# Kernel tuning notes

Measured on AMD Instinct MI355X. Metric: run time of the kernel, lower is better.

Reference implementation:

```python
import jax, jax.numpy as jnp
import numpy as np
import math

B, TQ, TK, C, H, DFF = 4, 1024, 1024, 1024, 16, 4096
DK = C // H
EPS = 1e-12


def _mha(x_q, x_kv, wq, bq, wk, bk, wv, bv, wo, bo, mask):
    Bq, Tq, Cq = x_q.shape
    Tk = x_kv.shape[1]
    q = (x_q @ wq + bq).reshape(Bq, Tq, H, DK).transpose(0, 2, 1, 3)  # [B,H,Tq,dk]
    k = (x_kv @ wk + bk).reshape(Bq, Tk, H, DK).transpose(0, 2, 1, 3)
    v = (x_kv @ wv + bv).reshape(Bq, Tk, H, DK).transpose(0, 2, 1, 3)
    scores = jnp.einsum('bhqd,bhkd->bhqk', q, k) * (1.0 / math.sqrt(DK))
    if mask is not None:
        scores = jnp.where(mask, scores, jnp.asarray(-1e9, scores.dtype))
    attn = jax.nn.softmax(scores, axis=-1)
    o = jnp.einsum('bhqk,bhkd->bhqd', attn, v).transpose(0, 2, 1, 3).reshape(Bq, Tq, Cq)
    return o @ wo + bo


def _ln(x, g, b):
    mu = jnp.mean(x, axis=-1, keepdims=True)
    var = jnp.mean(jnp.square(x - mu), axis=-1, keepdims=True)
    return (x - mu) * jax.lax.rsqrt(var + EPS) * g + b


def setup_inputs() -> dict:
    key = jax.random.key(0)
    ks = iter(jax.random.split(key, 32))
    s = 0.02
    inp = {}
    inp['src'] = jax.random.normal(next(ks), (B, TK, C), jnp.float32)
    inp['dst'] = jax.random.normal(next(ks), (B, TQ, C), jnp.float32)
    inp['src_mask'] = jnp.ones((B, 1, 1, TK), dtype=bool)  # key-padding mask (all valid)
    inp['dst_mask'] = jnp.tril(jnp.ones((TQ, TQ), dtype=bool))[None, None]  # causal
    for p in ['sa', 'ca']:
        for n in ['wq', 'wk', 'wv', 'wo']:
            inp[f'{p}_{n}'] = jax.random.normal(next(ks), (C, C), jnp.float32) * s
        for n in ['bq', 'bk', 'bv', 'bo']:
            inp[f'{p}_{n}'] = jnp.zeros((C,), jnp.float32)
    inp['ffn_w1'] = jax.random.normal(next(ks), (C, DFF), jnp.float32) * s
    inp['ffn_b1'] = jnp.zeros((DFF,), jnp.float32)
    inp['ffn_w2'] = jax.random.normal(next(ks), (DFF, C), jnp.float32) * s
    inp['ffn_b2'] = jnp.zeros((C,), jnp.float32)
    for i in ['1', '2', '3']:
        inp[f'ln{i}_g'] = jnp.ones((C,), jnp.float32)
        inp[f'ln{i}_b'] = jnp.zeros((C,), jnp.float32)
    return inp


def reference(src, dst, src_mask, dst_mask,
              sa_wq, sa_wk, sa_wv, sa_wo, sa_bq, sa_bk, sa_bv, sa_bo,
              ca_wq, ca_wk, ca_wv, ca_wo, ca_bq, ca_bk, ca_bv, ca_bo,
              ffn_w1, ffn_b1, ffn_w2, ffn_b2,
              ln1_g, ln1_b, ln2_g, ln2_b, ln3_g, ln3_b):
    # post-LN decoder layer, eval mode (dropout is identity)
    sa = _mha(dst, dst, sa_wq, sa_bq, sa_wk, sa_bk, sa_wv, sa_bv, sa_wo, sa_bo, dst_mask)
    y = _ln(dst + sa, ln1_g, ln1_b)
    ca = _mha(y, src, ca_wq, ca_bq, ca_wk, ca_bk, ca_wv, ca_bv, ca_wo, ca_bo, src_mask)
    y = _ln(y + ca, ln2_g, ln2_b)
    ff = jax.nn.gelu(y @ ffn_w1 + ffn_b1, approximate=False) @ ffn_w2 + ffn_b2
    return _ln(y + ff, ln3_g, ln3_b)
```

## Files before the change

kernel.cpp:

```cpp
#include <hip/hip_runtime.h>
#include <math.h>

typedef __attribute__((ext_vector_type(4))) float f32x4;
typedef __attribute__((ext_vector_type(8))) __bf16 bf16x8;
typedef __attribute__((ext_vector_type(8))) short short8;

#define DEV __device__ __forceinline__

DEV short f2bfs(float f) {
    unsigned u = __builtin_bit_cast(unsigned, f);
    unsigned r = (u + 0x7FFFu + ((u >> 16) & 1u)) >> 16;
    return (short)r;
}

DEV f32x4 mfma16(bf16x8 a, bf16x8 b, f32x4 c) {
    return __builtin_amdgcn_mfma_f32_16x16x32_bf16(a, b, c, 0, 0, 0);
}

DEV void gload_lds16(const void* g, void* l) {
    __builtin_amdgcn_global_load_lds((const __attribute__((address_space(1))) void*)g,
                                     (__attribute__((address_space(3))) void*)l, 16, 0, 0);
}

__global__ __launch_bounds__(256) void wtrans(const float* __restrict__ Win,
                                              short* __restrict__ Wout,
                                              int Kd, int Nd) {
    __shared__ float Tt[64][65];
    const int tx = threadIdx.x & 15, ty = threadIdx.x >> 4;
    const int k0 = blockIdx.y * 64, n0 = blockIdx.x * 64;
#pragma unroll
    for (int rr = 0; rr < 4; ++rr) {
        int k = ty + rr * 16;
        float4 v = *(const float4*)&Win[(size_t)(k0 + k) * Nd + n0 + tx * 4];
        Tt[k][tx * 4 + 0] = v.x; Tt[k][tx * 4 + 1] = v.y;
        Tt[k][tx * 4 + 2] = v.z; Tt[k][tx * 4 + 3] = v.w;
    }
    __syncthreads();
#pragma unroll
    for (int rr = 0; rr < 4; ++rr) {
        int n = ty + rr * 16;
        short4 o;
        o.x = f2bfs(Tt[tx * 4 + 0][n]);
        o.y = f2bfs(Tt[tx * 4 + 1][n]);
        o.z = f2bfs(Tt[tx * 4 + 2][n]);
        o.w = f2bfs(Tt[tx * 4 + 3][n]);
        *(short4*)&Wout[(size_t)(n0 + n) * Kd + k0 + tx * 4] = o;
    }
}

struct WPtrs { const float* p[8]; };

__global__ __launch_bounds__(256) void wtrans8(WPtrs wp, short* __restrict__ out) {
    const float* __restrict__ Win = wp.p[blockIdx.z];
    short* __restrict__ Wout = out + (size_t)blockIdx.z * (1024 * 1024);
    __shared__ float Tt[64][65];
    const int tx = threadIdx.x & 15, ty = threadIdx.x >> 4;
    const int k0 = blockIdx.y * 64, n0 = blockIdx.x * 64;
#pragma unroll
    for (int rr = 0; rr < 4; ++rr) {
        int k = ty + rr * 16;
        float4 v = *(const float4*)&Win[(size_t)(k0 + k) * 1024 + n0 + tx * 4];
        Tt[k][tx * 4 + 0] = v.x; Tt[k][tx * 4 + 1] = v.y;
        Tt[k][tx * 4 + 2] = v.z; Tt[k][tx * 4 + 3] = v.w;
    }
    __syncthreads();
#pragma unroll
    for (int rr = 0; rr < 4; ++rr) {
        int n = ty + rr * 16;
        short4 o;
        o.x = f2bfs(Tt[tx * 4 + 0][n]);
        o.y = f2bfs(Tt[tx * 4 + 1][n]);
        o.z = f2bfs(Tt[tx * 4 + 2][n]);
        o.w = f2bfs(Tt[tx * 4 + 3][n]);
        *(short4*)&Wout[(size_t)(n0 + n) * 1024 + k0 + tx * 4] = o;
    }
}

__global__ __launch_bounds__(256) void conv_bf16(const float* __restrict__ X,
                                                 short* __restrict__ Y, int n8) {
    int i = blockIdx.x * 256 + threadIdx.x;
    if (i < n8) {
        float4 a = ((const float4*)X)[i * 2];
        float4 b = ((const float4*)X)[i * 2 + 1];
        short8 o;
        o[0] = f2bfs(a.x); o[1] = f2bfs(a.y); o[2] = f2bfs(a.z); o[3] = f2bfs(a.w);
        o[4] = f2bfs(b.x); o[5] = f2bfs(b.y); o[6] = f2bfs(b.z); o[7] = f2bfs(b.w);
        ((short8*)Y)[i] = o;
    }
}

template <int BM, int BN, int BK, int EPI, int SWZ>
__global__ __launch_bounds__(256, (BM == 64 && BN == 64) ? 4 : 1)
void gemm_bt(const short* __restrict__ A,
             const short* __restrict__ BT,
             const float* __restrict__ b0,
             const float* __restrict__ b1,
             const float* __restrict__ b2,
             void* __restrict__ o0,
             void* __restrict__ o1,
             void* __restrict__ o2,
             int M, int N, int K, int Ks) {
    constexpr int IM = BM / 32, JN = BN / 32;
    constexpr int KH = BK / 32;
    constexpr int AL = (BM * 64) / 4096;
    constexpr int BL = (BN * 64) / 4096;
    __shared__ __align__(16) short As[2][BM * BK];
    __shared__ __align__(16) short Bs[2][BN * BK];
    const int tid = threadIdx.x, lane = tid & 63, w = tid >> 6;

    int bx, by, bz;
    if (SWZ == 1) {
        int gx = gridDim.x, gy = gridDim.y;
        int G = gx * gy * gridDim.z;
        int fid = blockIdx.x + gx * (blockIdx.y + gy * blockIdx.z);
        int nf = (fid & 7) * (G >> 3) + (fid >> 3);
        bx = nf % gx;
        int t = nf / gx;
        by = t % gy;
        bz = t / gy;
    } else if (SWZ == 2) {
        int gx = gridDim.x, gy = gridDim.y;
        int G = gx * gy * gridDim.z;
        int fid = blockIdx.x + gx * (blockIdx.y + gy * blockIdx.z);
        int nf = (fid & 7) * (G >> 3) + (fid >> 3);
        by = nf % gy;
        int t = nf / gy;
        bx = t % gx;
        bz = t / gx;
    } else {
        bx = blockIdx.x; by = blockIdx.y; bz = blockIdx.z;
    }

    const int m0 = by * BM, n0 = bx * BN;
    const int kz = bz * K;
    const int wm = (w & 1) * (BM / 2), wn = (w >> 1) * (BN / 2);
    const int rl = lane & 15, rg = lane >> 4;
    f32x4 acc[IM][JN] = {};
    const char* Ab = (const char*)A;
    const char* Bb = (const char*)BT;
    const int nk = K / BK;

    auto stage = [&](int kt, int buf) {
#pragma unroll
        for (int h = 0; h < KH; ++h) {
#pragma unroll
            for (int r = 0; r < AL; ++r) {
                int lo = (tid + r * 256) * 16;
                int row = lo >> 6, cp = (lo >> 4) & 3, c = (cp - (row >> 1)) & 3;
                gload_lds16(Ab + ((size_t)(m0 + row) * Ks + kz + kt * BK + h * 32 + c * 8) * 2,
                            (char*)As[buf] + h * (BM * 64) + lo);
            }
#pragma unroll
            for (int r = 0; r < BL; ++r) {
                int lo = (tid + r * 256) * 16;
                int row = lo >> 6, cp = (lo >> 4) & 3, c = (cp - (row >> 1)) & 3;
                gload_lds16(Bb + ((size_t)(n0 + row) * Ks + kz + kt * BK + h * 32 + c * 8) * 2,
                            (char*)Bs[buf] + h * (BN * 64) + lo);
            }
        }
    };

    stage(0, 0);
    for (int kt = 0; kt < nk; ++kt) {
        const int buf = kt & 1;
        __syncthreads();
        if (kt + 1 < nk) stage(kt + 1, buf ^ 1);
        bf16x8 af[KH][IM], bfr[KH][JN];
#pragma unroll
        for (int h = 0; h < KH; ++h) {
#pragma unroll
            for (int i = 0; i < IM; i++) {
                int row = wm + i * 16 + rl;
                af[h][i] = *(const bf16x8*)(As[buf] + h * (BM * 32) + row * 32 +
                                            ((rg + (row >> 1)) & 3) * 8);
            }
#pragma unroll
            for (int j = 0; j < JN; j++) {
                int row = wn + j * 16 + rl;
                bfr[h][j] = *(const bf16x8*)(Bs[buf] + h * (BN * 32) + row * 32 +
                                             ((rg + (row >> 1)) & 3) * 8);
            }
        }
#pragma unroll
        for (int h = 0; h < KH; ++h)
#pragma unroll
            for (int i = 0; i < IM; i++)
#pragma unroll
                for (int j = 0; j < JN; j++)
                    acc[i][j] = mfma16(af[h][i], bfr[h][j], acc[i][j]);
    }

    float* o0z = (float*)o0 + (size_t)bz * M * N;
#pragma unroll
    for (int i = 0; i < IM; i++) {
        int gm0 = m0 + wm + i * 16 + rg * 4;
#pragma unroll
        for (int j = 0; j < JN; j++) {
            int gn = n0 + wn + j * 16 + rl;
            if (EPI == 0) {
                float bv = bz == 0 ? b0[gn] : 0.0f;
#pragma unroll
                for (int r = 0; r < 4; r++)
                    o0z[(size_t)(gm0 + r) * N + gn] = acc[i][j][r] + bv;
            } else if (EPI == 2) {
                float bv = b0[gn];
#pragma unroll
                for (int r = 0; r < 4; r++) {
                    float x = acc[i][j][r] + bv;
                    float z = 1.59576912f * x + 0.07135481f * x * x * x;
                    float g = x / (1.0f + __expf(-z));
                    ((short*)o0)[(size_t)(gm0 + r) * N + gn] = f2bfs(g);
                }
            } else {
                int seg = gn >> 10, n1 = gn & 1023, h = n1 >> 6, d = n1 & 63;
                int b = gm0 >> 10, t0 = gm0 & 1023;
                bool isV = (EPI == 1) ? (seg == 2) : (seg == 1);
                const float* bp = (EPI == 1) ? (seg == 0 ? b0 : (seg == 1 ? b1 : b2))
                                             : (seg == 0 ? b0 : b1);
                float bv = bp[n1];
                float qs = (EPI == 1 && seg == 0) ? 0.125f : 1.0f;
                if (!isV) {
                    short* hp = (short*)((EPI == 1) ? (seg == 0 ? o0 : o1) : o0);
                    size_t base = ((size_t)(b * 16 + h) * 1024 + t0) * 64 + d;
#pragma unroll
                    for (int r = 0; r < 4; r++)
                        hp[base + (size_t)r * 64] = f2bfs((acc[i][j][r] + bv) * qs);
                } else {
                    short* vp = (short*)((EPI == 1) ? o2 : o1);
                    short4 pk;
                    pk.x = f2bfs(acc[i][j][0] + bv);
                    pk.y = f2bfs(acc[i][j][1] + bv);
                    pk.z = f2bfs(acc[i][j][2] + bv);
                    pk.w = f2bfs(acc[i][j][3] + bv);
                    *(short4*)(vp + ((size_t)(b * 16 + h) * 64 + d) * 1024 + t0) = pk;
                }
            }
        }
    }
}

template <bool CAUSAL>
__global__ __launch_bounds__(256, 3) void attn4(const short* __restrict__ Qh,
                                                const short* __restrict__ Kh,
                                                const short* __restrict__ VTh,
                                                short* __restrict__ Out, int TKn) {
    __shared__ __align__(16) short Ks[2][64 * 64];
    __shared__ __align__(16) short Vts[2][64 * 64];
    __shared__ __align__(16) short Ps[4][16 * 72 + 8];
    const int tid = threadIdx.x, lane = tid & 63, w = tid >> 6;
    const int rl = lane & 15, rg = lane >> 4;
    const int bh = blockIdx.y, b = bh >> 4, h = bh & 15;
    const int q0 = blockIdx.x * 64;
    const short* Qp = Qh + (size_t)bh * 1024 * 64;
    const char* Kp = (const char*)(Kh + (size_t)bh * (size_t)TKn * 64);
    const char* Vp = (const char*)(VTh + (size_t)bh * (size_t)TKn * 64);

    const int qrow = q0 + w * 16 + rl;
    const bf16x8 qf0 = *(const bf16x8*)(Qp + (size_t)qrow * 64 + rg * 8);
    const bf16x8 qf1 = *(const bf16x8*)(Qp + (size_t)qrow * 64 + 32 + rg * 8);

    bf16x8 onesf;
#pragma unroll
    for (int i = 0; i < 8; ++i) onesf[i] = (__bf16)1.0f;

    f32x4 o[4] = {};
    f32x4 lacc = {};

    short* Pw = &Ps[w][0];
    const int nkt = CAUSAL ? blockIdx.x + 1 : (TKn >> 6);

    auto stage = [&](int kt, int buf) {
#pragma unroll
        for (int r = 0; r < 2; ++r) {
            int lo = (w * 2 + r) * 1024 + lane * 16;
            int row = lo >> 7, cp = (lo >> 4) & 7, c = (cp - row) & 7;
            gload_lds16(Kp + ((size_t)(kt * 64 + row) * 64 + c * 8) * 2,
                        (char*)Ks[buf] + lo);
            gload_lds16(Vp + ((size_t)row * TKn + kt * 64 + c * 8) * 2,
                        (char*)Vts[buf] + lo);
        }
    };

    stage(0, 0);
    for (int kt = 0; kt < nkt; ++kt) {
        const int buf = kt & 1;
        __syncthreads();
        if (kt + 1 < nkt) stage(kt + 1, buf ^ 1);

        const short* KsB = Ks[buf];
        f32x4 s[4];
#pragma unroll
        for (int ch = 0; ch < 4; ++ch) {
            int row = ch * 16 + rl;
            bf16x8 k0 = *(const bf16x8*)(KsB + row * 64 + ((rg + row) & 7) * 8);
            bf16x8 k1 = *(const bf16x8*)(KsB + row * 64 + ((rg + 4 + row) & 7) * 8);
            f32x4 z = {};
            z = mfma16(k0, qf0, z);
            z = mfma16(k1, qf1, z);
            s[ch] = z;
        }
        const bool domask = CAUSAL && (kt == nkt - 1);
#pragma unroll
        for (int ch = 0; ch < 4; ++ch) {
            float p[4];
#pragma unroll
            for (int r = 0; r < 4; ++r) {
                float e = __expf(s[ch][r]);
                if (domask) {
                    int key = kt * 64 + ch * 16 + rg * 4 + r;
                    if (key > qrow) e = 0.0f;
                }
                p[r] = e;
            }
            unsigned d0 = (__builtin_bit_cast(unsigned, p[1]) & 0xFFFF0000u) |
                          (__builtin_bit_cast(unsigned, p[0]) >> 16);
            unsigned d1 = (__builtin_bit_cast(unsigned, p[3]) & 0xFFFF0000u) |
                          (__builtin_bit_cast(unsigned, p[2]) >> 16);
            uint2 dv; dv.x = d0; dv.y = d1;
            *(uint2*)(Pw + rl * 72 + ch * 16 + rg * 4) = dv;
        }
        bf16x8 pa0 = *(const bf16x8*)(Pw + rl * 72 + rg * 8);
        bf16x8 pa1 = *(const bf16x8*)(Pw + rl * 72 + 32 + rg * 8);
        lacc = mfma16(pa0, onesf, lacc);
        lacc = mfma16(pa1, onesf, lacc);
        const short* VsB = Vts[buf];
#pragma unroll
        for (int j = 0; j < 4; ++j) {
            int row = j * 16 + rl;
            bf16x8 v0 = *(const bf16x8*)(VsB + row * 64 + ((rg + row) & 7) * 8);
            bf16x8 v1 = *(const bf16x8*)(VsB + row * 64 + ((rg + 4 + row) & 7) * 8);
            o[j] = mfma16(pa0, v0, o[j]);
            o[j] = mfma16(pa1, v1, o[j]);
        }
    }

    float inv[4];
#pragma unroll
    for (int r = 0; r < 4; r++) inv[r] = 1.0f / lacc[r];
#pragma unroll
    for (int j = 0; j < 4; j++) {
#pragma unroll
        for (int r = 0; r < 4; r++) {
            int row = q0 + w * 16 + rg * 4 + r;
            int col = h * 64 + j * 16 + rl;
            Out[((size_t)b * 1024 + row) * 1024 + col] = f2bfs(o[j][r] * inv[r]);
        }
    }
}

__global__ __launch_bounds__(256) void ln_fused(const float* __restrict__ X,
                                                const float* __restrict__ R,
                                                const float* __restrict__ R2,
                                                const float* __restrict__ gam,
                                                const float* __restrict__ bet,
                                                float* __restrict__ Yf,
                                                short* __restrict__ Yb) {
    const int row = blockIdx.x, tid = threadIdx.x;
    const int lane = tid & 63, w = tid >> 6;
    float4 xv = ((const float4*)(X + (size_t)row * 1024))[tid];
    float4 rv = ((const float4*)(R + (size_t)row * 1024))[tid];
    float v0 = xv.x + rv.x, v1 = xv.y + rv.y, v2 = xv.z + rv.z, v3 = xv.w + rv.w;
    if (R2) {
        float4 r2 = ((const float4*)(R2 + (size_t)row * 1024))[tid];
        v0 += r2.x; v1 += r2.y; v2 += r2.z; v3 += r2.w;
    }
    float s = v0 + v1 + v2 + v3;
    float ss = v0 * v0 + v1 * v1 + v2 * v2 + v3 * v3;
#pragma unroll
    for (int off = 1; off < 64; off <<= 1) {
        s += __shfl_xor(s, off);
        ss += __shfl_xor(ss, off);
    }
    __shared__ float sred[4], ssred[4];
    if (lane == 0) { sred[w] = s; ssred[w] = ss; }
    __syncthreads();
    s = sred[0] + sred[1] + sred[2] + sred[3];
    ss = ssred[0] + ssred[1] + ssred[2] + ssred[3];
    float mu = s * (1.0f / 1024.0f);
    float var = ss * (1.0f / 1024.0f) - mu * mu;
    float rsq = rsqrtf(var + 1e-12f);
    float4 gv = ((const float4*)gam)[tid];
    float4 bv = ((const float4*)bet)[tid];
    float y0 = (v0 - mu) * rsq * gv.x + bv.x;
    float y1 = (v1 - mu) * rsq * gv.y + bv.y;
    float y2 = (v2 - mu) * rsq * gv.z + bv.z;
    float y3 = (v3 - mu) * rsq * gv.w + bv.w;
    float4 yo = {y0, y1, y2, y3};
    ((float4*)(Yf + (size_t)row * 1024))[tid] = yo;
    if (Yb) {
        short4 ob;
        ob.x = f2bfs(y0); ob.y = f2bfs(y1); ob.z = f2bfs(y2); ob.w = f2bfs(y3);
        ((short4*)(Yb + (size_t)row * 1024))[tid] = ob;
    }
}

extern "C" void kernel_launch(void* const* d_in, const int* in_sizes, int n_in,
                              void* d_out, int out_size, void* d_ws, size_t ws_size,
                              hipStream_t stream) {
    const float* src = (const float*)d_in[0];
    const float* dst = (const float*)d_in[1];
    const float* sa_wq = (const float*)d_in[4];
    const float* sa_wk = (const float*)d_in[5];
    const float* sa_wv = (const float*)d_in[6];
    const float* sa_wo = (const float*)d_in[7];
    const float* sa_bq = (const float*)d_in[8];
    const float* sa_bk = (const float*)d_in[9];
    const float* sa_bv = (const float*)d_in[10];
    const float* sa_bo = (const float*)d_in[11];
    const float* ca_wq = (const float*)d_in[12];
    const float* ca_wk = (const float*)d_in[13];
    const float* ca_wv = (const float*)d_in[14];
    const float* ca_wo = (const float*)d_in[15];
    const float* ca_bq = (const float*)d_in[16];
    const float* ca_bk = (const float*)d_in[17];
    const float* ca_bv = (const float*)d_in[18];
    const float* ca_bo = (const float*)d_in[19];
    const float* ffn_w1 = (const float*)d_in[20];
    const float* ffn_b1 = (const float*)d_in[21];
    const float* ffn_w2 = (const float*)d_in[22];
    const float* ffn_b2 = (const float*)d_in[23];
    const float* ln1g = (const float*)d_in[24];
    const float* ln1b = (const float*)d_in[25];
    const float* ln2g = (const float*)d_in[26];
    const float* ln2b = (const float*)d_in[27];
    const float* ln3g = (const float*)d_in[28];
    const float* ln3b = (const float*)d_in[29];

    char* ws = (char*)d_ws;
    size_t off = 0;
    auto alloc = [&](size_t n) { size_t o = off; off = (off + n + 255) & ~(size_t)255; return o; };

    const size_t szW = (size_t)1024 * 1024 * 2;
    short* wT = (short*)(ws + alloc(8 * szW));
    short* w1T = (short*)(ws + alloc((size_t)4096 * 1024 * 2));
    short* w2T = (short*)(ws + alloc((size_t)1024 * 4096 * 2));
    const size_t szAct2 = (size_t)4096 * 1024 * 2;
    const size_t szAct4 = (size_t)4096 * 1024 * 4;
    short* dstb = (short*)(ws + alloc(szAct2));
    short* srcb = (short*)(ws + alloc(szAct2));
    short* Qh = (short*)(ws + alloc(szAct2));
    short* Kh = (short*)(ws + alloc(szAct2));
    short* VTh = (short*)(ws + alloc(szAct2));
    short* attnb = (short*)(ws + alloc(szAct2));
    float* tmp = (float*)(ws + alloc(szAct4));
    float* y1f = (float*)(ws + alloc(szAct4));
    short* y1b = (short*)(ws + alloc(szAct2));
    float* y2f = (float*)(ws + alloc(szAct4));
    short* y2b = (short*)(ws + alloc(szAct2));
    short* ffnh = (short*)(ws + alloc((size_t)4096 * 4096 * 2));

    short* sa_wqkvT = wT;
    short* sa_woT = wT + 3 * (size_t)1048576;
    short* ca_wqT = wT + 4 * (size_t)1048576;
    short* ca_wkvT = wT + 5 * (size_t)1048576;
    short* ca_woT = wT + 7 * (size_t)1048576;

    dim3 blk(256);

    WPtrs wp = {{sa_wq, sa_wk, sa_wv, sa_wo, ca_wq, ca_wk, ca_wv, ca_wo}};
    wtrans8<<<dim3(16, 16, 8), blk, 0, stream>>>(wp, wT);
    wtrans<<<dim3(64, 16), blk, 0, stream>>>(ffn_w1, w1T, 1024, 4096);
    wtrans<<<dim3(16, 64), blk, 0, stream>>>(ffn_w2, w2T, 4096, 1024);
    conv_bf16<<<2048, blk, 0, stream>>>(dst, dstb, 524288);
    conv_bf16<<<2048, blk, 0, stream>>>(src, srcb, 524288);

    gemm_bt<128, 128, 32, 1, 2><<<dim3(24, 32), blk, 0, stream>>>(
        dstb, sa_wqkvT, sa_bq, sa_bk, sa_bv, Qh, Kh, VTh, 4096, 3072, 1024, 1024);
    attn4<true><<<dim3(16, 64), blk, 0, stream>>>(Qh, Kh, VTh, attnb, 1024);
    gemm_bt<64, 64, 64, 0, 2><<<dim3(16, 64), blk, 0, stream>>>(
        attnb, sa_woT, sa_bo, nullptr, nullptr, tmp, nullptr, nullptr, 4096, 1024, 1024, 1024);
    ln_fused<<<4096, blk, 0, stream>>>(dst, tmp, nullptr, ln1g, ln1b, y1f, y1b);

    gemm_bt<64, 64, 64, 1, 2><<<dim3(16, 64), blk, 0, stream>>>(
        y1b, ca_wqT, ca_bq, nullptr, nullptr, Qh, nullptr, nullptr, 4096, 1024, 1024, 1024);
    gemm_bt<128, 128, 32, 3, 2><<<dim3(16, 32), blk, 0, stream>>>(
        srcb, ca_wkvT, ca_bk, ca_bv, nullptr, Kh, VTh, nullptr, 4096, 2048, 1024, 1024);
    attn4<false><<<dim3(16, 64), blk, 0, stream>>>(Qh, Kh, VTh, attnb, 1024);
    gemm_bt<64, 64, 64, 0, 2><<<dim3(16, 64), blk, 0, stream>>>(
        attnb, ca_woT, ca_bo, nullptr, nullptr, tmp, nullptr, nullptr, 4096, 1024, 1024, 1024);
    ln_fused<<<4096, blk, 0, stream>>>(y1f, tmp, nullptr, ln2g, ln2b, y2f, y2b);

    gemm_bt<128, 128, 32, 2, 2><<<dim3(32, 32), blk, 0, stream>>>(
        y2b, w1T, ffn_b1, nullptr, nullptr, ffnh, nullptr, nullptr, 4096, 4096, 1024, 1024);
    gemm_bt<64, 64, 64, 0, 2><<<dim3(16, 64), blk, 0, stream>>>(
        ffnh, w2T, ffn_b2, nullptr, nullptr, tmp, nullptr, nullptr, 4096, 1024, 4096, 4096);
    ln_fused<<<4096, blk, 0, stream>>>(y2f, tmp, nullptr, ln3g, ln3b, (float*)d_out, nullptr);

    (void)in_sizes; (void)n_in; (void)out_size; (void)ws_size;
}
```

Before: 551.0 us.

## Load B fragments directly from global, reverse causal block order, retune swizzle/occupancy

Adds a BDIR path to the 64x64 GEMMs that reads weight fragments straight from global memory into registers and drops their LDS staging, which shrinks LDS use and raises the occupancy hint to 6. The causal attention kernel now schedules the longest query blocks first to balance load. The SWZ=2 swizzle is removed: the 128x128 GEMMs switch to no swizzle and the 64x64 ones to SWZ=1. Direct global B loads skip the double-buffered prefetch, so their latency is exposed and relies on the cache.

Measured after the change: 643.7 us. 16.8% more time.

```diff
diff --git a/kernel.cpp b/kernel.cpp
--- a/kernel.cpp
+++ b/kernel.cpp
@@ -89,8 +89,8 @@
     }
 }
 
-template <int BM, int BN, int BK, int EPI, int SWZ>
-__global__ __launch_bounds__(256, (BM == 64 && BN == 64) ? 4 : 1)
+template <int BM, int BN, int BK, int EPI, int SWZ, bool BDIR = false>
+__global__ __launch_bounds__(256, (BM == 64 && BN == 64) ? 6 : 1)
 void gemm_bt(const short* __restrict__ A,
              const short* __restrict__ BT,
              const float* __restrict__ b0,
@@ -105,7 +105,7 @@
     constexpr int AL = (BM * 64) / 4096;
     constexpr int BL = (BN * 64) / 4096;
     __shared__ __align__(16) short As[2][BM * BK];
-    __shared__ __align__(16) short Bs[2][BN * BK];
+    __shared__ __align__(16) short Bs[2][BDIR ? 8 : BN * BK];
     const int tid = threadIdx.x, lane = tid & 63, w = tid >> 6;
 
     int bx, by, bz;
@@ -118,15 +118,6 @@
         int t = nf / gx;
         by = t % gy;
         bz = t / gy;
-    } else if (SWZ == 2) {
-        int gx = gridDim.x, gy = gridDim.y;
-        int G = gx * gy * gridDim.z;
-        int fid = blockIdx.x + gx * (blockIdx.y + gy * blockIdx.z);
-        int nf = (fid & 7) * (G >> 3) + (fid >> 3);
-        by = nf % gy;
-        int t = nf / gy;
-        bx = t % gx;
-        bz = t / gx;
     } else {
         bx = blockIdx.x; by = blockIdx.y; bz = blockIdx.z;
     }
@@ -150,12 +141,14 @@
                 gload_lds16(Ab + ((size_t)(m0 + row) * Ks + kz + kt * BK + h * 32 + c * 8) * 2,
                             (char*)As[buf] + h * (BM * 64) + lo);
             }
-#pragma unroll
-            for (int r = 0; r < BL; ++r) {
-                int lo = (tid + r * 256) * 16;
-                int row = lo >> 6, cp = (lo >> 4) & 3, c = (cp - (row >> 1)) & 3;
-                gload_lds16(Bb + ((size_t)(n0 + row) * Ks + kz + kt * BK + h * 32 + c * 8) * 2,
-                            (char*)Bs[buf] + h * (BN * 64) + lo);
+            if constexpr (!BDIR) {
+#pragma unroll
+                for (int r = 0; r < BL; ++r) {
+                    int lo = (tid + r * 256) * 16;
+                    int row = lo >> 6, cp = (lo >> 4) & 3, c = (cp - (row >> 1)) & 3;
+                    gload_lds16(Bb + ((size_t)(n0 + row) * Ks + kz + kt * BK + h * 32 + c * 8) * 2,
+                                (char*)Bs[buf] + h * (BN * 64) + lo);
+                }
             }
         }
     };
@@ -177,8 +170,13 @@
 #pragma unroll
             for (int j = 0; j < JN; j++) {
                 int row = wn + j * 16 + rl;
-                bfr[h][j] = *(const bf16x8*)(Bs[buf] + h * (BN * 32) + row * 32 +
-                                             ((rg + (row >> 1)) & 3) * 8);
+                if constexpr (BDIR) {
+                    bfr[h][j] = *(const bf16x8*)(Bb + ((size_t)(n0 + row) * Ks + kz +
+                                                       kt * BK + h * 32 + rg * 8) * 2);
+                } else {
+                    bfr[h][j] = *(const bf16x8*)(Bs[buf] + h * (BN * 32) + row * 32 +
+                                                 ((rg + (row >> 1)) & 3) * 8);
+                }
             }
         }
 #pragma unroll
@@ -250,7 +248,8 @@
     const int tid = threadIdx.x, lane = tid & 63, w = tid >> 6;
     const int rl = lane & 15, rg = lane >> 4;
     const int bh = blockIdx.y, b = bh >> 4, h = bh & 15;
-    const int q0 = blockIdx.x * 64;
+    const int qb = CAUSAL ? (gridDim.x - 1 - blockIdx.x) : blockIdx.x;
+    const int q0 = qb * 64;
     const short* Qp = Qh + (size_t)bh * 1024 * 64;
     const char* Kp = (const char*)(Kh + (size_t)bh * (size_t)TKn * 64);
     const char* Vp = (const char*)(VTh + (size_t)bh * (size_t)TKn * 64);
@@ -267,7 +266,7 @@
     f32x4 lacc = {};
 
     short* Pw = &Ps[w][0];
-    const int nkt = CAUSAL ? blockIdx.x + 1 : (TKn >> 6);
+    const int nkt = CAUSAL ? qb + 1 : (TKn >> 6);
 
     auto stage = [&](int kt, int buf) {
 #pragma unroll
@@ -464,25 +463,25 @@
     conv_bf16<<<2048, blk, 0, stream>>>(dst, dstb, 524288);
     conv_bf16<<<2048, blk, 0, stream>>>(src, srcb, 524288);
 
-    gemm_bt<128, 128, 32, 1, 2><<<dim3(24, 32), blk, 0, stream>>>(
+    gemm_bt<128, 128, 32, 1, 0><<<dim3(24, 32), blk, 0, stream>>>(
         dstb, sa_wqkvT, sa_bq, sa_bk, sa_bv, Qh, Kh, VTh, 4096, 3072, 1024, 1024);
     attn4<true><<<dim3(16, 64), blk, 0, stream>>>(Qh, Kh, VTh, attnb, 1024);
-    gemm_bt<64, 64, 64, 0, 2><<<dim3(16, 64), blk, 0, stream>>>(
+    gemm_bt<64, 64, 64, 0, 1, true><<<dim3(16, 64), blk, 0, stream>>>(
         attnb, sa_woT, sa_bo, nullptr, nullptr, tmp, nullptr, nullptr, 4096, 1024, 1024, 1024);
     ln_fused<<<4096, blk, 0, stream>>>(dst, tmp, nullptr, ln1g, ln1b, y1f, y1b);
 
-    gemm_bt<64, 64, 64, 1, 2><<<dim3(16, 64), blk, 0, stream>>>(
+    gemm_bt<64, 64, 64, 1, 1, true><<<dim3(16, 64), blk, 0, stream>>>(
         y1b, ca_wqT, ca_bq, nullptr, nullptr, Qh, nullptr, nullptr, 4096, 1024, 1024, 1024);
-    gemm_bt<128, 128, 32, 3, 2><<<dim3(16, 32), blk, 0, stream>>>(
+    gemm_bt<128, 128, 32, 3, 0><<<dim3(16, 32), blk, 0, stream>>>(
         srcb, ca_wkvT, ca_bk, ca_bv, nullptr, Kh, VTh, nullptr, 4096, 2048, 1024, 1024);
     attn4<false><<<dim3(16, 64), blk, 0, stream>>>(Qh, Kh, VTh, attnb, 1024);
-    gemm_bt<64, 64, 64, 0, 2><<<dim3(16, 64), blk, 0, stream>>>(
+    gemm_bt<64, 64, 64, 0, 1, true><<<dim3(16, 64), blk, 0, stream>>>(
         attnb, ca_woT, ca_bo, nullptr, nullptr, tmp, nullptr, nullptr, 4096, 1024, 1024, 1024);
     ln_fused<<<4096, blk, 0, stream>>>(y1f, tmp, nullptr, ln2g, ln2b, y2f, y2b);
 
-    gemm_bt<128, 128, 32, 2, 2><<<dim3(32, 32), blk, 0, stream>>>(
+    gemm_bt<128, 128, 32, 2, 0><<<dim3(32, 32), blk, 0, stream>>>(
         y2b, w1T, ffn_b1, nullptr, nullptr, ffnh, nullptr, nullptr, 4096, 4096, 1024, 1024);
-    gemm_bt<64, 64, 64, 0, 2><<<dim3(16, 64), blk, 0, stream>>>(
+    gemm_bt<64, 64, 64, 0, 1, true><<<dim3(16, 64), blk, 0, stream>>>(
         ffnh, w2T, ffn_b2, nullptr, nullptr, tmp, nullptr, nullptr, 4096, 1024, 4096, 4096);
     ln_fused<<<4096, blk, 0, stream>>>(y2f, tmp, nullptr, ln3g, ln3b, (float*)d_out, nullptr);
 
```
